# Kernel optimization log

Measured on AMD Instinct MI355X. Metric: run time of the kernel, lower is better.

Reference implementation:

```python
import jax, jax.numpy as jnp
import numpy as np

B, T, D, H, E = 32, 512, 768, 12, 6  # batch, seq(=input_size), n_embd, num_heads, per-head dim
DFF = 4 * D
EPS = 1e-5


def setup_inputs() -> dict:
    key = jax.random.key(0)
    ks = jax.random.split(key, 10)
    s = 0.02
    return {
        "x": jax.random.normal(ks[0], (B, T, D), jnp.float32),
        "Wq": jax.random.normal(ks[1], (H, D, E), jnp.float32) * s,
        "Wk": jax.random.normal(ks[2], (H, D, E), jnp.float32) * s,
        "Wv": jax.random.normal(ks[3], (H, D, E), jnp.float32) * s,
        "Wo": jax.random.normal(ks[4], (H * E, D), jnp.float32) * s,
        "bo": jnp.zeros((D,), jnp.float32),
        "W1": jax.random.normal(ks[5], (D, DFF), jnp.float32) * s,
        "b1": jnp.zeros((DFF,), jnp.float32),
        "W2": jax.random.normal(ks[6], (DFF, D), jnp.float32) * s,
        "b2": jnp.zeros((D,), jnp.float32),
        "g1": jnp.ones((D,), jnp.float32),
        "beta1": jnp.zeros((D,), jnp.float32),
        "g2": jnp.ones((D,), jnp.float32),
        "beta2": jnp.zeros((D,), jnp.float32),
    }


def _layernorm(x, g, b):
    m = jnp.mean(x, axis=-1, keepdims=True)
    v = jnp.var(x, axis=-1, keepdims=True)  # biased, matches torch LayerNorm
    return (x - m) * jax.lax.rsqrt(v + EPS) * g + b


def reference(x, Wq, Wk, Wv, Wo, bo, W1, b1, W2, b2, g1, beta1, g2, beta2):
    # --- pre-LN multi-head causal attention (dropout = identity, eval mode) ---
    xn = _layernorm(x, g1, beta1)
    q = jnp.einsum("btd,hde->bhte", xn, Wq)
    k = jnp.einsum("btd,hde->bhte", xn, Wk)
    v = jnp.einsum("btd,hde->bhte", xn, Wv)
    scores = jnp.einsum("bhte,bhse->bhts", q, k) * (E ** -0.5)
    causal = jnp.tril(jnp.ones((T, T), dtype=bool))
    scores = jnp.where(causal, scores, -jnp.inf)
    w = jax.nn.softmax(scores, axis=-1)
    o = jnp.einsum("bhts,bhse->bhte", w, v)
    o = o.transpose(0, 2, 1, 3).reshape(B, T, H * E)  # concat heads -> [B,T,72]
    x = x + o @ Wo + bo
    # --- pre-LN feed-forward ---
    y = _layernorm(x, g2, beta2)
    ff = jax.nn.relu(y @ W1 + b1) @ W2 + b2
    return x + ff
```

## Files before the change

kernel.cpp:

```cpp
#include <hip/hip_runtime.h>
#include <hip/hip_bf16.h>

#define BT 16384
#define DIM 768
#define NH 12
#define DFF 3072

typedef __attribute__((ext_vector_type(8))) short short8;
typedef __attribute__((ext_vector_type(4))) float floatx4;
typedef __attribute__((ext_vector_type(4))) unsigned short ushort4b;

using bf16 = __hip_bfloat16;

static __device__ __forceinline__ float b2f(bf16 v) { return __bfloat162float(v); }
static __device__ __forceinline__ bf16 f2b(float v) { return __float2bfloat16(v); }

static __device__ __forceinline__ void gload_lds16(const void* g, void* l) {
    __builtin_amdgcn_global_load_lds(
        (const __attribute__((address_space(1))) unsigned int*)g,
        (__attribute__((address_space(3))) unsigned int*)l, 16, 0, 0);
}

__global__ __launch_bounds__(256) void pack_small_kernel(
    const float* __restrict__ Wq, const float* __restrict__ Wk, const float* __restrict__ Wv,
    const float* __restrict__ Wo, bf16* __restrict__ wqkv, bf16* __restrict__ wo_t)
{
    int i = blockIdx.x * 256 + threadIdx.x;
    const int S0 = 256 * 768, S1 = 768 * 96;
    if (i < S0) {
        int c = i / 768, dd = i % 768;
        float v = 0.f;
        if (c < 216) {
            int sel = c / 72, cc = c % 72, h = cc / 6, e = cc % 6;
            const float* W = (sel == 0) ? Wq : (sel == 1) ? Wk : Wv;
            v = W[((size_t)h * 768 + dd) * 6 + e];
        }
        wqkv[i] = f2b(v);
    } else if ((i -= S0) < S1) {
        int n = i / 96, r = i % 96;
        wo_t[i] = f2b(r < 72 ? Wo[r * 768 + n] : 0.f);
    }
}

__global__ __launch_bounds__(256) void transpose_kernel(
    const float* __restrict__ in, bf16* __restrict__ out, int R, int C)
{
    __shared__ float t[32][33];
    int c0 = blockIdx.x * 32, r0 = blockIdx.y * 32;
    int cx = threadIdx.x & 31, ry = threadIdx.x >> 5;
#pragma unroll
    for (int j = 0; j < 4; j++)
        t[ry + j * 8][cx] = in[(size_t)(r0 + ry + j * 8) * C + c0 + cx];
    __syncthreads();
    int rx = cx, cy = ry;
#pragma unroll
    for (int j = 0; j < 4; j++)
        out[(size_t)(c0 + cy + j * 8) * R + r0 + rx] = f2b(t[rx][cy + j * 8]);
}

__global__ __launch_bounds__(192) void ln_kernel(
    const float* __restrict__ x, const float* __restrict__ g, const float* __restrict__ be,
    bf16* __restrict__ out)
{
    int row = blockIdx.x;
    int tid = threadIdx.x;
    const float4* xr = (const float4*)(x + (size_t)row * DIM);
    float4 v = xr[tid];
    float s = v.x + v.y + v.z + v.w;
    float s2 = v.x * v.x + v.y * v.y + v.z * v.z + v.w * v.w;
#pragma unroll
    for (int off = 32; off; off >>= 1) {
        s += __shfl_down(s, off);
        s2 += __shfl_down(s2, off);
    }
    __shared__ float red[6];
    int wv = tid >> 6, ln = tid & 63;
    if (ln == 0) { red[wv] = s; red[3 + wv] = s2; }
    __syncthreads();
    float ts = red[0] + red[1] + red[2];
    float ts2 = red[3] + red[4] + red[5];
    float mean = ts * (1.f / 768.f);
    float var = ts2 * (1.f / 768.f) - mean * mean;
    float rstd = rsqrtf(var + 1e-5f);
    int c = tid * 4;
    float o0 = (v.x - mean) * rstd * g[c + 0] + be[c + 0];
    float o1 = (v.y - mean) * rstd * g[c + 1] + be[c + 1];
    float o2 = (v.z - mean) * rstd * g[c + 2] + be[c + 2];
    float o3 = (v.w - mean) * rstd * g[c + 3] + be[c + 3];
    bf16 h0 = f2b(o0), h1 = f2b(o1), h2 = f2b(o2), h3 = f2b(o3);
    ushort4b pk;
    pk[0] = *(unsigned short*)&h0; pk[1] = *(unsigned short*)&h1;
    pk[2] = *(unsigned short*)&h2; pk[3] = *(unsigned short*)&h3;
    *(ushort4b*)(out + (size_t)row * DIM + c) = pk;
}

template <int NSLAB, bool RELU, bool BIAS, bool RES, bool BF16OUT>
__global__ __launch_bounds__(256) void gemm_kernel(
    const bf16* __restrict__ A, const bf16* __restrict__ Bt,
    const float* __restrict__ bias, const float* __restrict__ res,
    void* __restrict__ Cv, int M, int N, int K)
{
    constexpr int SMEM_BYTES = BF16OUT ? (128 * 136 * 2) : (NSLAB * 2 * 128 * 32 * 2);
    __shared__ __align__(16) char smem[SMEM_BYTES];
    bf16* lA = (bf16*)smem;
    bf16* lB = lA + NSLAB * 128 * 32;

    const int tid = threadIdx.x;
    const int bm = blockIdx.x * 128;
    const int bn = blockIdx.y * 128;
    const int wave = tid >> 6, lane = tid & 63;
    const int wm = (wave >> 1) * 64, wn = (wave & 1) * 64;
    const int quad = lane >> 4, l16 = lane & 15;
    const int lrow = lane >> 2;
    const int lkc = (lane & 3) * 8;

    floatx4 acc[4][4] = {};

    for (int k0 = 0; k0 < K; k0 += NSLAB * 32) {
#pragma unroll
        for (int s = 0; s < NSLAB; s++) {
#pragma unroll
            for (int it = 0; it < 2; it++) {
                int r = wave * 32 + it * 16;
                gload_lds16(A + (size_t)(bm + r + lrow) * K + k0 + s * 32 + lkc,
                            lA + s * 4096 + r * 32);
                gload_lds16(Bt + (size_t)(bn + r + lrow) * K + k0 + s * 32 + lkc,
                            lB + s * 4096 + r * 32);
            }
        }
        __syncthreads();
#pragma unroll
        for (int s = 0; s < NSLAB; s++) {
            short8 af[4], bfr[4];
#pragma unroll
            for (int mt = 0; mt < 4; mt++)
                af[mt] = *(const short8*)(lA + s * 4096 + (wm + mt * 16 + l16) * 32 + quad * 8);
#pragma unroll
            for (int nt = 0; nt < 4; nt++)
                bfr[nt] = *(const short8*)(lB + s * 4096 + (wn + nt * 16 + l16) * 32 + quad * 8);
#pragma unroll
            for (int mt = 0; mt < 4; mt++)
#pragma unroll
                for (int nt = 0; nt < 4; nt++)
                    acc[mt][nt] = __builtin_amdgcn_mfma_f32_16x16x32_bf16(af[mt], bfr[nt], acc[mt][nt], 0, 0, 0);
        }
        __syncthreads();
    }

    if constexpr (BF16OUT) {
        bf16* ltile = (bf16*)smem;
#pragma unroll
        for (int mt = 0; mt < 4; mt++) {
#pragma unroll
            for (int nt = 0; nt < 4; nt++) {
                int tc = wn + nt * 16 + l16;
#pragma unroll
                for (int r = 0; r < 4; r++) {
                    int tr = wm + mt * 16 + quad * 4 + r;
                    float v0 = acc[mt][nt][r];
                    if constexpr (BIAS) v0 += bias[bn + tc];
                    if constexpr (RELU) v0 = fmaxf(v0, 0.f);
                    ltile[tr * 136 + tc] = f2b(v0);
                }
            }
        }
        __syncthreads();
        bf16* C = (bf16*)Cv;
        int rr0 = tid >> 4, col8 = (tid & 15) * 8;
        int gc = bn + col8;
#pragma unroll
        for (int p = 0; p < 8; p++) {
            int rr = p * 16 + rr0;
            if (gc < N)
                *(short8*)(C + (size_t)(bm + rr) * N + gc) =
                    *(const short8*)(ltile + rr * 136 + col8);
        }
    } else {
        float* C = (float*)Cv;
#pragma unroll
        for (int mt = 0; mt < 4; mt++) {
#pragma unroll
            for (int nt = 0; nt < 4; nt++) {
                int gc = bn + wn + nt * 16 + l16;
                if (gc < N) {
#pragma unroll
                    for (int r = 0; r < 4; r++) {
                        int gr = bm + wm + mt * 16 + quad * 4 + r;
                        float v0 = acc[mt][nt][r];
                        if constexpr (BIAS) v0 += bias[gc];
                        if constexpr (RES) v0 += res[(size_t)gr * N + gc];
                        if constexpr (RELU) v0 = fmaxf(v0, 0.f);
                        C[(size_t)gr * N + gc] = v0;
                    }
                }
            }
        }
    }
}

template <bool RELU, bool BIAS, bool RES, bool BF16OUT>
__global__ __launch_bounds__(512, 2) void gemm256_kernel(
    const bf16* __restrict__ A, const bf16* __restrict__ Bt,
    const float* __restrict__ bias, const float* __restrict__ res,
    void* __restrict__ Cv, int M, int N, int K)
{
    extern __shared__ __align__(16) char smem[];
    const int NT = K >> 6;
    const int nbm = M >> 8;
    const int nwg = nbm * (N >> 8);
    int idx = blockIdx.x;
    idx = (idx & 7) * (nwg >> 3) + (idx >> 3);
    const int bm = (idx % nbm) << 8;
    const int bn = (idx / nbm) << 8;

    const int tid = threadIdx.x;
    const int w = tid >> 6, lane = tid & 63;
    const int wm = w >> 2, wn = w & 3;
    const int l16 = lane & 15, quad = lane >> 4;

    const int rstg = (w >> 1) * 16 + (lane >> 2);
    const int cstg = (w & 1) * 32 + ((((lane & 3) * 8)) ^ ((lane & 32) ? 16 : 0));
    const bf16* aSrc = A + (size_t)(bm + rstg) * K + cstg;
    const bf16* bSrc = Bt + (size_t)(bn + rstg) * K + cstg;
    char* dstBase = smem + w * 1024;

    const int xr = (quad * 16) ^ ((l16 & 8) ? 32 : 0);
    const int aOff = wm * 16384 + l16 * 64 + xr;
    const int bOff = 32768 + wn * 8192 + l16 * 64 + xr;

#define STAGE(P, ISB, H, T) { \
    const bf16* _s = ((ISB) ? bSrc : aSrc) + ((size_t)((H) * 128) * K + (size_t)(T) * 64); \
    char* _d = dstBase + (P) * 65536 + (ISB) * 32768 + (H) * 16384; \
    gload_lds16(_s, _d); \
    gload_lds16(_s + (size_t)64 * K, _d + 8192); }

#define BARX() asm volatile("s_barrier" ::: "memory")
#define VMW(N_) asm volatile("s_waitcnt vmcnt(" #N_ ")" ::: "memory")

    floatx4 acc[8][4] = {};
    short8 a[4][2], b[2][2][2];

#define LDA(QM, CB) { _Pragma("unroll") for (int fm = 0; fm < 4; fm++) { \
    _Pragma("unroll") for (int s = 0; s < 2; s++) \
        a[fm][s] = *(const short8*)((CB) + aOff + (QM) * 8192 + fm * 2048 + s * 1024); } }
#define LDB(QN, CB) { _Pragma("unroll") for (int fn = 0; fn < 2; fn++) { \
    _Pragma("unroll") for (int s = 0; s < 2; s++) \
        b[QN][fn][s] = *(const short8*)((CB) + bOff + (QN) * 4096 + fn * 2048 + s * 1024); } }
#define MM(QM, QN) { __builtin_amdgcn_s_setprio(1); \
    _Pragma("unroll") for (int fm = 0; fm < 4; fm++) { \
    _Pragma("unroll") for (int fn = 0; fn < 2; fn++) { \
    _Pragma("unroll") for (int s = 0; s < 2; s++) \
        acc[(QM)*4+fm][(QN)*2+fn] = __builtin_amdgcn_mfma_f32_16x16x32_bf16( \
            a[fm][s], b[QN][fn][s], acc[(QM)*4+fm][(QN)*2+fn], 0, 0, 0); } } \
    __builtin_amdgcn_s_setprio(0); }

    STAGE(0, 1, 0, 0); STAGE(0, 1, 1, 0); STAGE(0, 0, 0, 0); STAGE(0, 0, 1, 0);
    STAGE(1, 1, 0, 1); STAGE(1, 1, 1, 1); STAGE(1, 0, 0, 1);
    VMW(6);
    BARX();

    for (int g = 0; g < NT; ++g) {
        const int p = g & 1, pn = p ^ 1;
        const char* cb = smem + p * 65536;
        LDA(0, cb); LDB(0, cb);
        if (g + 1 < NT) STAGE(pn, 0, 1, g + 1);
        BARX(); MM(0, 0); BARX();
        LDB(1, cb);
        if (g + 2 < NT) STAGE(p, 1, 0, g + 2);
        BARX(); MM(0, 1); BARX();
        LDA(1, cb);
        if (g + 2 < NT) STAGE(p, 1, 1, g + 2);
        BARX(); MM(1, 0); BARX();
        if (g + 2 < NT) STAGE(p, 0, 0, g + 2);
        BARX(); MM(1, 1);
        if (g < NT - 2) { VMW(6); } else { VMW(0); }
        BARX();
    }

    if constexpr (BF16OUT) {
        bf16* lt = (bf16*)smem;
#pragma unroll
        for (int RF = 0; RF < 8; RF++) {
            const int row = wm * 128 + (RF >> 2) * 64 + (RF & 3) * 16 + quad * 4;
#pragma unroll
            for (int CF = 0; CF < 4; CF++) {
                const int col = wn * 64 + (CF >> 1) * 32 + (CF & 1) * 16 + l16;
                float bv = BIAS ? bias[bn + col] : 0.f;
#pragma unroll
                for (int rr = 0; rr < 4; rr++) {
                    float v = acc[RF][CF][rr] + bv;
                    if constexpr (RELU) v = fmaxf(v, 0.f);
                    lt[(row + rr) * 280 + col] = f2b(v);
                }
            }
        }
        asm volatile("s_waitcnt lgkmcnt(0)" ::: "memory");
        BARX();
        bf16* C = (bf16*)Cv;
#pragma unroll
        for (int it = 0; it < 16; it++) {
            int c = it * 512 + tid;
            int rr = c >> 5, c8 = (c & 31) * 8;
            *(short8*)(C + (size_t)(bm + rr) * N + bn + c8) =
                *(const short8*)(lt + rr * 280 + c8);
        }
    } else {
        float* C = (float*)Cv;
#pragma unroll
        for (int RF = 0; RF < 8; RF++) {
            const int gr = bm + wm * 128 + (RF >> 2) * 64 + (RF & 3) * 16 + quad * 4;
#pragma unroll
            for (int CF = 0; CF < 4; CF++) {
                const int gc = bn + wn * 64 + (CF >> 1) * 32 + (CF & 1) * 16 + l16;
                float bv = BIAS ? bias[gc] : 0.f;
#pragma unroll
                for (int rr = 0; rr < 4; rr++) {
                    float v = acc[RF][CF][rr] + bv;
                    if constexpr (RES) v += res[(size_t)(gr + rr) * N + gc];
                    if constexpr (RELU) v = fmaxf(v, 0.f);
                    C[(size_t)(gr + rr) * N + gc] = v;
                }
            }
        }
    }
#undef STAGE
#undef BARX
#undef VMW
#undef LDA
#undef LDB
#undef MM
}

__global__ __launch_bounds__(256) void attn_kernel(const bf16* __restrict__ qkv, bf16* __restrict__ o_pad)
{
    int blk = blockIdx.x;
    int half = blk & 1;
    int bh = blk >> 1;
    int b = bh / NH, h = bh % NH;
    int wave = threadIdx.x >> 6, lane = threadIdx.x & 63;
    const int jmap0[4] = {0, 2, 5, 7}, jmap1[4] = {1, 3, 4, 6};
    int j = half ? jmap1[wave] : jmap0[wave];
    int t = j * 64 + lane;
    int smax = half ? 448 : 512;

    __shared__ float ks[512 * 6];
    __shared__ float vs[512 * 6];
    const bf16* base = qkv + (size_t)b * 512 * 216;
    for (int i = threadIdx.x; i < smax * 6; i += 256) {
        int s = i / 6, e = i % 6;
        ks[i] = b2f(base[s * 216 + 72 + h * 6 + e]);
        vs[i] = b2f(base[s * 216 + 144 + h * 6 + e]);
    }
    __syncthreads();

    float q0 = b2f(base[t * 216 + h * 6 + 0]);
    float q1 = b2f(base[t * 216 + h * 6 + 1]);
    float q2 = b2f(base[t * 216 + h * 6 + 2]);
    float q3 = b2f(base[t * 216 + h * 6 + 3]);
    float q4 = b2f(base[t * 216 + h * 6 + 4]);
    float q5 = b2f(base[t * 216 + h * 6 + 5]);

    const float scale = 0.4082482904638630f;
    float m = -1e30f, l = 0.f;
    float o0 = 0, o1 = 0, o2 = 0, o3 = 0, o4 = 0, o5 = 0;
    for (int s = 0; s <= t; s++) {
        const float* kk = &ks[s * 6];
        float sc = (q0 * kk[0] + q1 * kk[1] + q2 * kk[2] + q3 * kk[3] + q4 * kk[4] + q5 * kk[5]) * scale;
        float nm = fmaxf(m, sc);
        float alpha = __expf(m - nm);
        float p = __expf(sc - nm);
        l = l * alpha + p;
        const float* vv = &vs[s * 6];
        o0 = o0 * alpha + p * vv[0];
        o1 = o1 * alpha + p * vv[1];
        o2 = o2 * alpha + p * vv[2];
        o3 = o3 * alpha + p * vv[3];
        o4 = o4 * alpha + p * vv[4];
        o5 = o5 * alpha + p * vv[5];
        m = nm;
    }
    float inv = 1.f / l;
    bf16* orow = o_pad + (size_t)(b * 512 + t) * 96 + h * 6;
    orow[0] = f2b(o0 * inv);
    orow[1] = f2b(o1 * inv);
    orow[2] = f2b(o2 * inv);
    orow[3] = f2b(o3 * inv);
    orow[4] = f2b(o4 * inv);
    orow[5] = f2b(o5 * inv);
}

extern "C" void kernel_launch(void* const* d_in, const int* in_sizes, int n_in,
                              void* d_out, int out_size, void* d_ws, size_t ws_size,
                              hipStream_t stream)
{
    const float* x   = (const float*)d_in[0];
    const float* Wq  = (const float*)d_in[1];
    const float* Wk  = (const float*)d_in[2];
    const float* Wv  = (const float*)d_in[3];
    const float* Wo  = (const float*)d_in[4];
    const float* bo  = (const float*)d_in[5];
    const float* W1  = (const float*)d_in[6];
    const float* b1  = (const float*)d_in[7];
    const float* W2  = (const float*)d_in[8];
    const float* b2  = (const float*)d_in[9];
    const float* g1  = (const float*)d_in[10];
    const float* be1 = (const float*)d_in[11];
    const float* g2  = (const float*)d_in[12];
    const float* be2 = (const float*)d_in[13];

    char* ws = (char*)d_ws;
    size_t off = 0;
    auto alloc = [&](size_t bytes) {
        void* p = ws + off;
        off = (off + bytes + 255) & ~(size_t)255;
        return p;
    };
    bf16*  xn    = (bf16*)alloc((size_t)BT * DIM * 2);
    bf16*  qkvb  = (bf16*)alloc((size_t)BT * 216 * 2);
    bf16*  o_pad = (bf16*)alloc((size_t)BT * 96 * 2);
    float* x1    = (float*)alloc((size_t)BT * DIM * 4);
    bf16*  ffb   = (bf16*)alloc((size_t)BT * DFF * 2);
    bf16*  wqkv  = (bf16*)alloc((size_t)256 * 768 * 2);
    bf16*  wo_t  = (bf16*)alloc((size_t)768 * 96 * 2);
    bf16*  w1t   = (bf16*)alloc((size_t)3072 * 768 * 2);
    bf16*  w2t   = (bf16*)alloc((size_t)768 * 3072 * 2);

    hipFuncSetAttribute(reinterpret_cast<const void*>(&gemm256_kernel<true, true, false, true>),
                        hipFuncAttributeMaxDynamicSharedMemorySize, 256 * 280 * 2);
    hipFuncSetAttribute(reinterpret_cast<const void*>(&gemm256_kernel<false, true, true, false>),
                        hipFuncAttributeMaxDynamicSharedMemorySize, 131072);

    const int PACK_N = 256 * 768 + 768 * 96;
    pack_small_kernel<<<(PACK_N + 255) / 256, 256, 0, stream>>>(Wq, Wk, Wv, Wo, wqkv, wo_t);
    transpose_kernel<<<dim3(3072 / 32, 768 / 32), 256, 0, stream>>>(W1, w1t, 768, 3072);
    transpose_kernel<<<dim3(768 / 32, 3072 / 32), 256, 0, stream>>>(W2, w2t, 3072, 768);

    ln_kernel<<<BT, 192, 0, stream>>>(x, g1, be1, xn);
    gemm_kernel<2, false, false, false, true><<<dim3(128, 2), 256, 0, stream>>>(
        xn, wqkv, nullptr, nullptr, qkvb, BT, 216, 768);
    attn_kernel<<<32 * NH * 2, 256, 0, stream>>>(qkvb, o_pad);
    gemm_kernel<1, false, true, true, false><<<dim3(128, 6), 256, 0, stream>>>(
        o_pad, wo_t, bo, x, x1, BT, 768, 96);
    ln_kernel<<<BT, 192, 0, stream>>>(x1, g2, be2, xn);
    gemm256_kernel<true, true, false, true><<<768, 512, 256 * 280 * 2, stream>>>(
        xn, w1t, b1, nullptr, ffb, BT, 3072, 768);
    gemm256_kernel<false, true, true, false><<<192, 512, 131072, stream>>>(
        ffb, w2t, b2, x1, (float*)d_out, BT, 768, 3072);
}
```

Measured before the change: 444.7 us.

## Switch FFN GEMMs from 256x256 to 256x192 tiles with reworked staging

The two large FFN GEMMs now use a 256x192 output tile instead of 256x256, with a 4x2 wave layout, new LDS staging offsets and a reordered MFMA/prefetch schedule. The aim is better wave-quantization across the CUs: 1024 and 256 workgroups instead of 768 and 192, which matters most for the 192-block second GEMM that may leave CUs idle. In exchange, each tile has a smaller arithmetic-intensity ratio, so per-FLOP operand loads rise. The epilogue is adapted to a 200-element LDS pitch.

```diff
diff --git a/kernel.cpp b/kernel.cpp
--- a/kernel.cpp
+++ b/kernel.cpp
@@ -199,7 +199,7 @@
 }
 
 template <bool RELU, bool BIAS, bool RES, bool BF16OUT>
-__global__ __launch_bounds__(512, 2) void gemm256_kernel(
+__global__ __launch_bounds__(512, 2) void gemm192_kernel(
     const bf16* __restrict__ A, const bf16* __restrict__ Bt,
     const float* __restrict__ bias, const float* __restrict__ res,
     void* __restrict__ Cv, int M, int N, int K)
@@ -207,123 +207,125 @@
     extern __shared__ __align__(16) char smem[];
     const int NT = K >> 6;
     const int nbm = M >> 8;
-    const int nwg = nbm * (N >> 8);
+    const int nwg = nbm * (N / 192);
     int idx = blockIdx.x;
     idx = (idx & 7) * (nwg >> 3) + (idx >> 3);
     const int bm = (idx % nbm) << 8;
-    const int bn = (idx / nbm) << 8;
+    const int bn = (idx / nbm) * 192;
 
     const int tid = threadIdx.x;
     const int w = tid >> 6, lane = tid & 63;
-    const int wm = w >> 2, wn = w & 3;
+    const int wm = w >> 1, wn = w & 1;
     const int l16 = lane & 15, quad = lane >> 4;
 
     const int rstg = (w >> 1) * 16 + (lane >> 2);
-    const int cstg = (w & 1) * 32 + ((((lane & 3) * 8)) ^ ((lane & 32) ? 16 : 0));
+    const int cstg = (w & 1) * 32 + (((lane & 3) * 8) ^ ((lane & 32) ? 16 : 0));
     const bf16* aSrc = A + (size_t)(bm + rstg) * K + cstg;
     const bf16* bSrc = Bt + (size_t)(bn + rstg) * K + cstg;
-    char* dstBase = smem + w * 1024;
+    const int stgoff = w * 1024;
 
     const int xr = (quad * 16) ^ ((l16 & 8) ? 32 : 0);
-    const int aOff = wm * 16384 + l16 * 64 + xr;
-    const int bOff = 32768 + wn * 8192 + l16 * 64 + xr;
-
-#define STAGE(P, ISB, H, T) { \
-    const bf16* _s = ((ISB) ? bSrc : aSrc) + ((size_t)((H) * 128) * K + (size_t)(T) * 64); \
-    char* _d = dstBase + (P) * 65536 + (ISB) * 32768 + (H) * 16384; \
-    gload_lds16(_s, _d); \
-    gload_lds16(_s + (size_t)64 * K, _d + 8192); }
+    const int aoff = wm * 8192 + l16 * 64 + xr;
+    const int boff = 32768 + wn * 12288 + l16 * 64 + xr;
+
+#define STG(BO, ISB, CH, T) gload_lds16( \
+        ((ISB) ? bSrc : aSrc) + (size_t)(CH) * 64 * K + (size_t)(T) * 64, \
+        smem + (BO) + (ISB) * 32768 + (CH) * 8192 + stgoff)
 
 #define BARX() asm volatile("s_barrier" ::: "memory")
 #define VMW(N_) asm volatile("s_waitcnt vmcnt(" #N_ ")" ::: "memory")
 
-    floatx4 acc[8][4] = {};
-    short8 a[4][2], b[2][2][2];
-
-#define LDA(QM, CB) { _Pragma("unroll") for (int fm = 0; fm < 4; fm++) { \
+    floatx4 acc[4][6] = {};
+    short8 a[2][2][2], b[3][2];
+
+#define LDA(QM, CB) { _Pragma("unroll") for (int fm = 0; fm < 2; fm++) { \
     _Pragma("unroll") for (int s = 0; s < 2; s++) \
-        a[fm][s] = *(const short8*)((CB) + aOff + (QM) * 8192 + fm * 2048 + s * 1024); } }
-#define LDB(QN, CB) { _Pragma("unroll") for (int fn = 0; fn < 2; fn++) { \
+        a[QM][fm][s] = *(const short8*)((CB) + aoff + (QM) * 4096 + fm * 2048 + s * 1024); } }
+#define LDB(QN, CB) { _Pragma("unroll") for (int fn = 0; fn < 3; fn++) { \
     _Pragma("unroll") for (int s = 0; s < 2; s++) \
-        b[QN][fn][s] = *(const short8*)((CB) + bOff + (QN) * 4096 + fn * 2048 + s * 1024); } }
+        b[fn][s] = *(const short8*)((CB) + boff + (QN) * 6144 + fn * 2048 + s * 1024); } }
 #define MM(QM, QN) { __builtin_amdgcn_s_setprio(1); \
-    _Pragma("unroll") for (int fm = 0; fm < 4; fm++) { \
-    _Pragma("unroll") for (int fn = 0; fn < 2; fn++) { \
+    _Pragma("unroll") for (int fm = 0; fm < 2; fm++) { \
+    _Pragma("unroll") for (int fn = 0; fn < 3; fn++) { \
     _Pragma("unroll") for (int s = 0; s < 2; s++) \
-        acc[(QM)*4+fm][(QN)*2+fn] = __builtin_amdgcn_mfma_f32_16x16x32_bf16( \
-            a[fm][s], b[QN][fn][s], acc[(QM)*4+fm][(QN)*2+fn], 0, 0, 0); } } \
+        acc[(QM)*2+fm][(QN)*3+fn] = __builtin_amdgcn_mfma_f32_16x16x32_bf16( \
+            a[QM][fm][s], b[fn][s], acc[(QM)*2+fm][(QN)*3+fn], 0, 0, 0); } } \
     __builtin_amdgcn_s_setprio(0); }
 
-    STAGE(0, 1, 0, 0); STAGE(0, 1, 1, 0); STAGE(0, 0, 0, 0); STAGE(0, 0, 1, 0);
-    STAGE(1, 1, 0, 1); STAGE(1, 1, 1, 1); STAGE(1, 0, 0, 1);
-    VMW(6);
+#pragma unroll
+    for (int c = 0; c < 4; c++) STG(0, 0, c, 0);
+#pragma unroll
+    for (int c = 0; c < 3; c++) STG(0, 1, c, 0);
+#pragma unroll
+    for (int c = 0; c < 4; c++) STG(57344, 0, c, 1);
+#pragma unroll
+    for (int c = 0; c < 3; c++) STG(57344, 1, c, 1);
+    VMW(7);
     BARX();
 
     for (int g = 0; g < NT; ++g) {
-        const int p = g & 1, pn = p ^ 1;
-        const char* cb = smem + p * 65536;
+        const int bo = (g & 1) * 57344;
+        const char* cb = smem + bo;
         LDA(0, cb); LDB(0, cb);
-        if (g + 1 < NT) STAGE(pn, 0, 1, g + 1);
         BARX(); MM(0, 0); BARX();
+        LDA(1, cb);
+        BARX(); MM(1, 0); BARX();
         LDB(1, cb);
-        if (g + 2 < NT) STAGE(p, 1, 0, g + 2);
-        BARX(); MM(0, 1); BARX();
-        LDA(1, cb);
-        if (g + 2 < NT) STAGE(p, 1, 1, g + 2);
-        BARX(); MM(1, 0); BARX();
-        if (g + 2 < NT) STAGE(p, 0, 0, g + 2);
-        BARX(); MM(1, 1);
-        if (g < NT - 2) { VMW(6); } else { VMW(0); }
+        if (g + 2 < NT) { STG(bo, 0, 0, g + 2); STG(bo, 0, 1, g + 2);
+                          STG(bo, 0, 2, g + 2); STG(bo, 0, 3, g + 2); }
+        BARX(); MM(1, 1); BARX();
+        if (g + 2 < NT) { STG(bo, 1, 0, g + 2); STG(bo, 1, 1, g + 2); STG(bo, 1, 2, g + 2); }
+        BARX(); MM(0, 1);
+        if (g < NT - 2) { VMW(7); } else { VMW(0); }
         BARX();
     }
 
     if constexpr (BF16OUT) {
         bf16* lt = (bf16*)smem;
 #pragma unroll
-        for (int RF = 0; RF < 8; RF++) {
-            const int row = wm * 128 + (RF >> 2) * 64 + (RF & 3) * 16 + quad * 4;
-#pragma unroll
-            for (int CF = 0; CF < 4; CF++) {
-                const int col = wn * 64 + (CF >> 1) * 32 + (CF & 1) * 16 + l16;
+        for (int mf = 0; mf < 4; mf++) {
+            const int row = wm * 64 + mf * 16 + quad * 4;
+#pragma unroll
+            for (int nf = 0; nf < 6; nf++) {
+                const int col = wn * 96 + nf * 16 + l16;
                 float bv = BIAS ? bias[bn + col] : 0.f;
 #pragma unroll
-                for (int rr = 0; rr < 4; rr++) {
-                    float v = acc[RF][CF][rr] + bv;
+                for (int r = 0; r < 4; r++) {
+                    float v = acc[mf][nf][r] + bv;
                     if constexpr (RELU) v = fmaxf(v, 0.f);
-                    lt[(row + rr) * 280 + col] = f2b(v);
+                    lt[(row + r) * 200 + col] = f2b(v);
                 }
             }
         }
-        asm volatile("s_waitcnt lgkmcnt(0)" ::: "memory");
-        BARX();
+        __syncthreads();
         bf16* C = (bf16*)Cv;
 #pragma unroll
-        for (int it = 0; it < 16; it++) {
+        for (int it = 0; it < 12; it++) {
             int c = it * 512 + tid;
-            int rr = c >> 5, c8 = (c & 31) * 8;
-            *(short8*)(C + (size_t)(bm + rr) * N + bn + c8) =
-                *(const short8*)(lt + rr * 280 + c8);
+            int rr = c / 24, cc = (c - rr * 24) * 8;
+            *(short8*)(C + (size_t)(bm + rr) * N + bn + cc) =
+                *(const short8*)(lt + rr * 200 + cc);
         }
     } else {
         float* C = (float*)Cv;
 #pragma unroll
-        for (int RF = 0; RF < 8; RF++) {
-            const int gr = bm + wm * 128 + (RF >> 2) * 64 + (RF & 3) * 16 + quad * 4;
-#pragma unroll
-            for (int CF = 0; CF < 4; CF++) {
-                const int gc = bn + wn * 64 + (CF >> 1) * 32 + (CF & 1) * 16 + l16;
+        for (int mf = 0; mf < 4; mf++) {
+            const int gr = bm + wm * 64 + mf * 16 + quad * 4;
+#pragma unroll
+            for (int nf = 0; nf < 6; nf++) {
+                const int gc = bn + wn * 96 + nf * 16 + l16;
                 float bv = BIAS ? bias[gc] : 0.f;
 #pragma unroll
-                for (int rr = 0; rr < 4; rr++) {
-                    float v = acc[RF][CF][rr] + bv;
-                    if constexpr (RES) v += res[(size_t)(gr + rr) * N + gc];
+                for (int r = 0; r < 4; r++) {
+                    float v = acc[mf][nf][r] + bv;
+                    if constexpr (RES) v += res[(size_t)(gr + r) * N + gc];
                     if constexpr (RELU) v = fmaxf(v, 0.f);
-                    C[(size_t)(gr + rr) * N + gc] = v;
+                    C[(size_t)(gr + r) * N + gc] = v;
                 }
             }
         }
     }
-#undef STAGE
+#undef STG
 #undef BARX
 #undef VMW
 #undef LDA
@@ -425,10 +427,10 @@
     bf16*  w1t   = (bf16*)alloc((size_t)3072 * 768 * 2);
     bf16*  w2t   = (bf16*)alloc((size_t)768 * 3072 * 2);
 
-    hipFuncSetAttribute(reinterpret_cast<const void*>(&gemm256_kernel<true, true, false, true>),
-                        hipFuncAttributeMaxDynamicSharedMemorySize, 256 * 280 * 2);
-    hipFuncSetAttribute(reinterpret_cast<const void*>(&gemm256_kernel<false, true, true, false>),
-                        hipFuncAttributeMaxDynamicSharedMemorySize, 131072);
+    hipFuncSetAttribute(reinterpret_cast<const void*>(&gemm192_kernel<true, true, false, true>),
+                        hipFuncAttributeMaxDynamicSharedMemorySize, 114688);
+    hipFuncSetAttribute(reinterpret_cast<const void*>(&gemm192_kernel<false, true, true, false>),
+                        hipFuncAttributeMaxDynamicSharedMemorySize, 114688);
 
     const int PACK_N = 256 * 768 + 768 * 96;
     pack_small_kernel<<<(PACK_N + 255) / 256, 256, 0, stream>>>(Wq, Wk, Wv, Wo, wqkv, wo_t);
@@ -442,8 +444,8 @@
     gemm_kernel<1, false, true, true, false><<<dim3(128, 6), 256, 0, stream>>>(
         o_pad, wo_t, bo, x, x1, BT, 768, 96);
     ln_kernel<<<BT, 192, 0, stream>>>(x1, g2, be2, xn);
-    gemm256_kernel<true, true, false, true><<<768, 512, 256 * 280 * 2, stream>>>(
+    gemm192_kernel<true, true, false, true><<<1024, 512, 114688, stream>>>(
         xn, w1t, b1, nullptr, ffb, BT, 3072, 768);
-    gemm256_kernel<false, true, true, false><<<192, 512, 131072, stream>>>(
+    gemm192_kernel<false, true, true, false><<<256, 512, 114688, stream>>>(
         ffb, w2t, b2, x1, (float*)d_out, BT, 768, 3072);
 }
```

Result: no change. 453.4 us (+2.0%).
